# Kernel tuning notes

Measured on AMD Instinct MI355X. Metric: run time of the kernel, lower is better.

The kernel has to match this reference:

```python
import jax, jax.numpy as jnp
import numpy as np

AABB0 = np.array([-1.5, -1.5, -1.5], np.float32)
AABB1 = np.array([1.5, 1.5, 1.5], np.float32)
GRID = (300, 300, 300)
NEAR, FAR = 2.0, 6.0
STEP = float(np.mean((AABB1 - AABB0) / (np.array(GRID, np.float32) - 1)) * 0.5)  # step_ratio=0.5
DIST_SCALE = 25.0
DENSITY_SHIFT = -10.0
W_THRES = 1e-4
PE = 2  # view_pe = feat_pe = 2
MAT = ((0, 1), (0, 2), (1, 2))
VEC = (2, 1, 0)
N_RAYS, N_SAMP = 1024, 512
DN, AN = 16, 16
APP_DIM, FEAT_C = 27, 128
IN_MLP = 2 * PE * 3 + 2 * PE * APP_DIM + 3 + APP_DIM  # 150


def posenc(x, freqs):
    fb = (2.0 ** jnp.arange(freqs)).astype(x.dtype)
    p = (x[..., None] * fb).reshape(x.shape[:-1] + (x.shape[-1] * freqs,))
    return jnp.concatenate([jnp.sin(p), jnp.cos(p)], -1)


def bilinear2d(plane, xy):
    # plane [C,H,W]; xy [P,2] in [-1,1], x->W, y->H; align_corners=True, border clamp
    C, H, W = plane.shape
    x = jnp.clip((xy[:, 0] * 0.5 + 0.5) * (W - 1), 0.0, W - 1)
    y = jnp.clip((xy[:, 1] * 0.5 + 0.5) * (H - 1), 0.0, H - 1)
    x0 = jnp.clip(jnp.floor(x), 0, W - 2).astype(jnp.int32)
    y0 = jnp.clip(jnp.floor(y), 0, H - 2).astype(jnp.int32)
    wx, wy = x - x0, y - y0
    v00 = plane[:, y0, x0]
    v01 = plane[:, y0, x0 + 1]
    v10 = plane[:, y0 + 1, x0]
    v11 = plane[:, y0 + 1, x0 + 1]
    return (v00 * (1 - wx) + v01 * wx) * (1 - wy) + (v10 * (1 - wx) + v11 * wx) * wy  # [C,P]


def linear1d(line, z):
    # line [C,L]; z [P] in [-1,1]
    C, L = line.shape
    t = jnp.clip((z * 0.5 + 0.5) * (L - 1), 0.0, L - 1)
    i0 = jnp.clip(jnp.floor(t), 0, L - 2).astype(jnp.int32)
    w = t - i0
    return line[:, i0] * (1 - w) + line[:, i0 + 1] * w  # [C,P]


def _forward(rays_o, rays_d, dplanes, dlines, aplanes, alines, basis_w,
             w1, b1, w2, b2, w3, b3, n_samples):
    a0, a1 = jnp.asarray(AABB0), jnp.asarray(AABB1)
    # --- sample_ray (is_train=False) ---
    vec = jnp.where(rays_d == 0, 1e-6, rays_d)
    rate_a = (a1 - rays_o) / vec
    rate_b = (a0 - rays_o) / vec
    t_min = jnp.clip(jnp.max(jnp.minimum(rate_a, rate_b), -1), NEAR, FAR)  # [R]
    rng = jnp.arange(n_samples, dtype=rays_o.dtype)[None]
    z_vals = t_min[:, None] + STEP * rng  # [R,S]
    pts = rays_o[:, None, :] + rays_d[:, None, :] * z_vals[..., None]  # [R,S,3]
    ray_valid = jnp.all((pts >= a0) & (pts <= a1), -1)  # [R,S]
    xn = ((pts - a0) * (2.0 / (a1 - a0)) - 1.0).reshape(-1, 3)  # normalize_coord -> [P,3]
    # --- density: VM decomposition (sum of plane*line products) ---
    sigma_feat = jnp.zeros((xn.shape[0],), xn.dtype)
    for i in range(3):
        p = bilinear2d(dplanes[i], xn[:, jnp.array(MAT[i])])
        l = linear1d(dlines[i], xn[:, VEC[i]])
        sigma_feat = sigma_feat + jnp.sum(p * l, 0)
    sigma = jax.nn.softplus(sigma_feat + DENSITY_SHIFT).reshape(z_vals.shape)
    sigma = jnp.where(ray_valid, sigma, 0.0)
    # --- raw2alpha compositing ---
    dists = jnp.concatenate([z_vals[:, 1:] - z_vals[:, :-1], jnp.zeros_like(z_vals[:, :1])], -1)
    alpha = 1.0 - jnp.exp(-sigma * dists * DIST_SCALE)
    T = jnp.cumprod(jnp.concatenate([jnp.ones_like(alpha[:, :1]), 1.0 - alpha + 1e-10], -1), -1)
    weight = alpha * T[:, :-1]
    app_mask = weight > W_THRES
    # --- appearance features + basis_mat ---
    coefs = [bilinear2d(aplanes[i], xn[:, jnp.array(MAT[i])]) * linear1d(alines[i], xn[:, VEC[i]])
             for i in range(3)]
    feat = jnp.concatenate(coefs, 0).T @ basis_w.T  # [P, app_dim]
    view = jnp.broadcast_to(rays_d[:, None, :], pts.shape).reshape(-1, 3)
    # --- MLPRender_Fea: [features, viewdirs, posenc(features), posenc(viewdirs)] ---
    mlp_in = jnp.concatenate([feat, view, posenc(feat, PE), posenc(view, PE)], -1)
    h = jax.nn.relu(mlp_in @ w1.T + b1)
    h = jax.nn.relu(h @ w2.T + b2)
    rgb = jax.nn.sigmoid(h @ w3.T + b3).reshape(z_vals.shape + (3,))
    rgb = jnp.where(app_mask[..., None], rgb, 0.0)
    acc = jnp.sum(weight, -1)
    rgb_map = jnp.sum(weight[..., None] * rgb, 1)
    rgb_map = jnp.clip(rgb_map + (1.0 - acc)[:, None], 0.0, 1.0)  # white background
    depth_map = jnp.sum(weight * z_vals, -1)
    return rgb_map, depth_map


def setup_inputs() -> dict:
    key = jax.random.key(0)
    ks = jax.random.split(key, 20)
    rd = jax.random.normal(ks[0], (N_RAYS, 3), jnp.float32)
    rays_d = rd / jnp.linalg.norm(rd, axis=-1, keepdims=True)
    rays_o = -3.0 * rays_d + 0.1 * jax.random.normal(ks[1], (N_RAYS, 3), jnp.float32)
    inp = {"rays_o": rays_o, "rays_d": rays_d}
    for i, ((m0, m1), v) in enumerate(zip(MAT, VEC)):
        inp[f"dplane{i}"] = jax.random.normal(ks[2 + i], (DN, GRID[m1], GRID[m0]), jnp.float32)
        inp[f"dline{i}"] = jax.random.normal(ks[5 + i], (DN, GRID[v]), jnp.float32)
        inp[f"aplane{i}"] = 0.1 * jax.random.normal(ks[8 + i], (AN, GRID[m1], GRID[m0]), jnp.float32)
        inp[f"aline{i}"] = 0.1 * jax.random.normal(ks[11 + i], (AN, GRID[v]), jnp.float32)
    inp["basis_w"] = 0.1 * jax.random.normal(ks[14], (APP_DIM, 3 * AN), jnp.float32)
    inp["w1"] = 0.05 * jax.random.normal(ks[15], (FEAT_C, IN_MLP), jnp.float32)
    inp["b1"] = jnp.zeros((FEAT_C,), jnp.float32)
    inp["w2"] = 0.05 * jax.random.normal(ks[16], (FEAT_C, FEAT_C), jnp.float32)
    inp["b2"] = jnp.zeros((FEAT_C,), jnp.float32)
    inp["w3"] = 0.05 * jax.random.normal(ks[17], (3, FEAT_C), jnp.float32)
    inp["b3"] = jnp.zeros((3,), jnp.float32)
    inp["n_samples"] = N_SAMP
    return inp


def reference(rays_o, rays_d, dplane0, dplane1, dplane2, dline0, dline1, dline2,
              aplane0, aplane1, aplane2, aline0, aline1, aline2, basis_w,
              w1, b1, w2, b2, w3, b3, n_samples):
    return _forward(rays_o, rays_d, (dplane0, dplane1, dplane2), (dline0, dline1, dline2),
                    (aplane0, aplane1, aplane2), (aline0, aline1, aline2), basis_w,
                    w1, b1, w2, b2, w3, b3, n_samples)
```

## Files before the change

kernel.cpp:

```cpp
#include <hip/hip_runtime.h>
#include <hip/hip_fp16.h>
#include <math.h>

#define NRAYS 1024
#define NSAMP 512
#define GRIDN 300
#define POS_ELEMS (GRIDN*GRIDN)
#define PLANE_ELEMS (16*POS_ELEMS)
#define CMAX 524288

typedef short bf16x8 __attribute__((ext_vector_type(8)));
typedef short short8 __attribute__((ext_vector_type(8)));
typedef float f32x4  __attribute__((ext_vector_type(4)));

struct H8v { __half2 h[4]; };

__device__ __forceinline__ float clampf(float x, float a, float b){ return fminf(fmaxf(x,a),b); }
__device__ __forceinline__ unsigned short f2b(float f){
    unsigned u = __builtin_bit_cast(unsigned, f);
    u = (u + 0x7FFFu + ((u>>16)&1u)) >> 16;
    return (unsigned short)u;
}
__device__ __forceinline__ float b2f(unsigned short h){
    unsigned u = ((unsigned)h) << 16;
    return __builtin_bit_cast(float, u);
}

__device__ __forceinline__ float ray_tmin(float o0,float o1,float o2,float d0,float d1,float d2){
    float v0=(d0==0.f)?1e-6f:d0, v1=(d1==0.f)?1e-6f:d1, v2=(d2==0.f)?1e-6f:d2;
    float t_min = -1e30f, a, b;
    a=(1.5f-o0)/v0; b=(-1.5f-o0)/v0; t_min=fmaxf(t_min,fminf(a,b));
    a=(1.5f-o1)/v1; b=(-1.5f-o1)/v1; t_min=fmaxf(t_min,fminf(a,b));
    a=(1.5f-o2)/v2; b=(-1.5f-o2)/v2; t_min=fmaxf(t_min,fminf(a,b));
    return clampf(t_min, 2.0f, 6.0f);
}

struct TPtrs {
    const float* psrc[6]; __half* pdst[6];
    const float* lsrc[6]; __half* ldst[6];
};

__global__ __launch_bounds__(256) void k_transpose(TPtrs tp) {
    int by  = blockIdx.y;
    int pos = blockIdx.x * 256 + threadIdx.x;
    if (pos < POS_ELEMS) {
        const float* src = tp.psrc[by];
        __half2 o[8];
        #pragma unroll
        for (int e = 0; e < 8; e++) {
            float a = src[(2*e  ) * POS_ELEMS + pos];
            float b = src[(2*e+1) * POS_ELEMS + pos];
            o[e] = __float22half2_rn(make_float2(a,b));
        }
        float4* dst = (float4*)(tp.pdst[by] + (size_t)pos * 16);
        dst[0] = *(float4*)&o[0];
        dst[1] = *(float4*)&o[4];
    }
    if (pos < GRIDN) {
        const float* ls = tp.lsrc[by];
        __half*      ld = tp.ldst[by];
        #pragma unroll
        for (int c = 0; c < 16; c++) ld[pos * 16 + c] = __float2half_rn(ls[c * GRIDN + pos]);
    }
}

__global__ __launch_bounds__(256) void k_prepw(
    const float* __restrict__ w1, const float* __restrict__ w2,
    unsigned short* __restrict__ w1b, unsigned short* __restrict__ w2b)
{
    int idx = blockIdx.x * 256 + threadIdx.x;
    if (idx < 128*160) {
        int j = idx / 160, k = idx - j*160;
        w1b[idx] = (k < 150) ? f2b(w1[j*150 + k]) : 0;
    } else if (idx < 128*160 + 128*128) {
        int i2 = idx - 128*160;
        w2b[i2] = f2b(w2[i2]);
    }
}

__global__ __launch_bounds__(256) void k_alpha(
    const float* __restrict__ ro, const float* __restrict__ rd,
    const __half* __restrict__ dpT0, const __half* __restrict__ dpT1, const __half* __restrict__ dpT2,
    const __half* __restrict__ dlT0, const __half* __restrict__ dlT1, const __half* __restrict__ dlT2,
    float* __restrict__ alpha_out)
{
    const float STEPF = (3.0f/299.0f)*0.5f;
    int gid = blockIdx.x*256 + threadIdx.x;
    int id = gid >> 1, h = gid & 1;
    int r = id >> 9, s = id & (NSAMP-1);

    float o0=ro[r*3+0], o1=ro[r*3+1], o2=ro[r*3+2];
    float d0=rd[r*3+0], d1=rd[r*3+1], d2=rd[r*3+2];
    float t_min = ray_tmin(o0,o1,o2,d0,d1,d2);

    float z  = t_min + STEPF * (float)s;
    float p0 = o0 + d0*z, p1 = o1 + d1*z, p2 = o2 + d2*z;
    bool valid = (p0>=-1.5f)&&(p0<=1.5f)&&(p1>=-1.5f)&&(p1<=1.5f)&&(p2>=-1.5f)&&(p2<=1.5f);

    float sfp = 0.f;
    if (valid) {
        float xn[3] = { (p0+1.5f)*(2.0f/3.0f)-1.0f,
                        (p1+1.5f)*(2.0f/3.0f)-1.0f,
                        (p2+1.5f)*(2.0f/3.0f)-1.0f };
        const __half* dpT[3] = {dpT0,dpT1,dpT2};
        const __half* dlT[3] = {dlT0,dlT1,dlT2};
        const int M0[3]={0,0,1}, M1[3]={1,2,2}, V[3]={2,1,0};
        #pragma unroll
        for (int i=0;i<3;i++) {
            float fx = clampf((xn[M0[i]]*0.5f+0.5f)*299.f, 0.f, 299.f);
            float fy = clampf((xn[M1[i]]*0.5f+0.5f)*299.f, 0.f, 299.f);
            float ft = clampf((xn[V[i]] *0.5f+0.5f)*299.f, 0.f, 299.f);
            int x0=min((int)fx,298), y0=min((int)fy,298), i0=min((int)ft,298);
            float wx=fx-(float)x0, wy=fy-(float)y0, wt=ft-(float)i0;
            __half2 w00=__float2half2_rn((1.f-wx)*(1.f-wy)), w01=__float2half2_rn(wx*(1.f-wy));
            __half2 w10=__float2half2_rn((1.f-wx)*wy),       w11=__float2half2_rn(wx*wy);
            __half2 u0 =__float2half2_rn(1.f-wt),            u1 =__float2half2_rn(wt);
            const __half* base = dpT[i] + (size_t)(y0*GRIDN+x0)*16 + h*8;
            H8v a00 = *(const H8v*)(base);
            H8v a01 = *(const H8v*)(base + 16);
            H8v a10 = *(const H8v*)(base + GRIDN*16);
            H8v a11 = *(const H8v*)(base + GRIDN*16 + 16);
            const __half* lb = dlT[i] + (size_t)i0*16 + h*8;
            H8v l0 = *(const H8v*)(lb);
            H8v l1 = *(const H8v*)(lb + 16);
            #pragma unroll
            for (int e=0;e<4;e++) {
                __half2 p = __hmul2(a00.h[e],w00);
                p = __hfma2(a01.h[e],w01,p);
                p = __hfma2(a10.h[e],w10,p);
                p = __hfma2(a11.h[e],w11,p);
                __half2 l = __hmul2(l0.h[e],u0);
                l = __hfma2(l1.h[e],u1,l);
                float2 c = __half22float2(__hmul2(p,l));
                sfp += c.x + c.y;
            }
        }
    }
    float sf = sfp + __shfl_xor(sfp, 1, 64);
    if (h == 0) {
        float sig = 0.f;
        if (valid) {
            float xs = sf - 10.0f;
            sig = fmaxf(xs, 0.f) + __logf(1.f + __expf(-fabsf(xs)));
        }
        alpha_out[id] = (s < NSAMP-1) ? (1.f - __expf(-sig * (STEPF*25.0f))) : 0.f;
    }
}

__global__ __launch_bounds__(256) void k_scan(
    const float* __restrict__ ro, const float* __restrict__ rd,
    const float* __restrict__ alpha_in,
    float* __restrict__ acc_out, float* __restrict__ depth_out,
    int* __restrict__ tmpl, float* __restrict__ tmpw, int* __restrict__ cnt)
{
    const float STEPF = (3.0f/299.0f)*0.5f;
    int r = blockIdx.x;
    int tid = threadIdx.x;
    int lane = tid & 63, wv = tid >> 6;

    float o0=ro[r*3+0], o1=ro[r*3+1], o2=ro[r*3+2];
    float d0=rd[r*3+0], d1=rd[r*3+1], d2=rd[r*3+2];
    float t_min = ray_tmin(o0,o1,o2,d0,d1,d2);

    float2 av = *(const float2*)&alpha_in[r*NSAMP + 2*tid];
    float aj0 = av.x, aj1 = av.y;
    float zj0 = t_min + STEPF * (float)(2*tid);
    float zj1 = t_min + STEPF * (float)(2*tid+1);

    float v0 = (1.f - aj0) + 1e-10f;
    float v1 = (1.f - aj1) + 1e-10f;
    float inc = v0 * v1;
    #pragma unroll
    for (int off=1; off<64; off<<=1) {
        float t = __shfl_up(inc, off, 64);
        if (lane >= off) inc *= t;
    }
    __shared__ float wtot[4], swsum[4], sdep[4];
    __shared__ int   wcnt[4];
    if (lane == 63) wtot[wv] = inc;
    __syncthreads();
    float pre = 1.f;
    for (int i=0;i<wv;i++) pre *= wtot[i];
    float excl = __shfl_up(inc, 1, 64);
    if (lane == 0) excl = 1.f;
    float T0 = pre * excl;
    float w0 = aj0 * T0;
    float w1 = aj1 * T0 * v0;

    float rw = w0 + w1, rz = w0*zj0 + w1*zj1;
    #pragma unroll
    for (int off=32; off>0; off>>=1) { rw += __shfl_xor(rw,off,64); rz += __shfl_xor(rz,off,64); }
    if (lane == 0) { swsum[wv] = rw; sdep[wv] = rz; }

    bool act0 = (w0 > 1e-4f), act1 = (w1 > 1e-4f);
    unsigned long long m0 = __ballot(act0);
    unsigned long long m1 = __ballot(act1);
    int tot = __popcll(m0) + __popcll(m1);
    if (lane == 0) wcnt[wv] = tot;
    __syncthreads();
    int base = 0;
    for (int i=0;i<wv;i++) base += wcnt[i];
    unsigned long long below = (1ull<<lane)-1ull;
    int o = base + __popcll(m0 & below) + __popcll(m1 & below);
    int* tl = tmpl + r*NSAMP;
    float* tw = tmpw + r*NSAMP;
    if (act0) { tl[o] = (r<<9)|(2*tid);   tw[o] = w0; o++; }
    if (act1) { tl[o] = (r<<9)|(2*tid+1); tw[o] = w1; }

    if (tid == 0) {
        float a=0.f, b=0.f;
        #pragma unroll
        for (int i=0;i<4;i++){ a+=swsum[i]; b+=sdep[i]; }
        acc_out[r] = a; depth_out[r] = b;
        cnt[r] = wcnt[0]+wcnt[1]+wcnt[2]+wcnt[3];
    }
}

__global__ __launch_bounds__(1024) void k_prefix(
    const int* __restrict__ cnt, int* __restrict__ basep, int* __restrict__ counter)
{
    int tid = threadIdx.x;
    int lane = tid & 63, wv = tid >> 6;
    int v = cnt[tid];
    int inc = v;
    #pragma unroll
    for (int off=1; off<64; off<<=1) {
        int t = __shfl_up(inc, off, 64);
        if (lane >= off) inc += t;
    }
    __shared__ int wsum[16];
    if (lane == 63) wsum[wv] = inc;
    __syncthreads();
    int pre = 0;
    for (int i=0;i<wv;i++) pre += wsum[i];
    basep[tid] = pre + inc - v;
    if (tid == 1023) *counter = pre + inc;
}

__global__ __launch_bounds__(256) void k_compact(
    const int* __restrict__ tmpl, const float* __restrict__ tmpw,
    const int* __restrict__ cnt, const int* __restrict__ basep,
    int* __restrict__ list, float* __restrict__ wlist)
{
    int r = blockIdx.x;
    int n = cnt[r], b = basep[r];
    const int* tl = tmpl + r*NSAMP;
    const float* tw = tmpw + r*NSAMP;
    for (int j = threadIdx.x; j < n; j += 256) {
        list[b+j]  = tl[j];
        wlist[b+j] = tw[j];
    }
}

__global__ __launch_bounds__(256) void k_gather(
    const float* __restrict__ ro, const float* __restrict__ rd,
    const __half* __restrict__ apT0, const __half* __restrict__ apT1, const __half* __restrict__ apT2,
    const __half* __restrict__ alT0, const __half* __restrict__ alT1, const __half* __restrict__ alT2,
    const float* __restrict__ basis_w,
    const int* __restrict__ list, const int* __restrict__ counter,
    float* __restrict__ Xf)
{
    const float STEPF = (3.0f/299.0f)*0.5f;
    int gid = blockIdx.x*256 + threadIdx.x;
    int idx = gid >> 3, q = gid & 7;
    int count = *counter;
    if (idx >= count) return;

    int sid = list[idx];
    int r = sid >> 9, s = sid & (NSAMP-1);
    float o0=ro[r*3+0], o1=ro[r*3+1], o2=ro[r*3+2];
    float d0=rd[r*3+0], d1=rd[r*3+1], d2=rd[r*3+2];
    float t_min = ray_tmin(o0,o1,o2,d0,d1,d2);
    float z = t_min + STEPF*(float)s;
    float xn[3] = { ((o0+d0*z)+1.5f)*(2.0f/3.0f)-1.0f,
                    ((o1+d1*z)+1.5f)*(2.0f/3.0f)-1.0f,
                    ((o2+d2*z)+1.5f)*(2.0f/3.0f)-1.0f };

    bool active = (q < 6);
    int i = min(q >> 1, 2);
    int h = q & 1;

    float c8[8];
    {
        const __half* apT[3]={apT0,apT1,apT2};
        const __half* alT[3]={alT0,alT1,alT2};
        const int M0[3]={0,0,1}, M1[3]={1,2,2}, V[3]={2,1,0};
        float fx = clampf((xn[M0[i]]*0.5f+0.5f)*299.f, 0.f, 299.f);
        float fy = clampf((xn[M1[i]]*0.5f+0.5f)*299.f, 0.f, 299.f);
        float ft = clampf((xn[V[i]] *0.5f+0.5f)*299.f, 0.f, 299.f);
        int x0=min((int)fx,298), y0=min((int)fy,298), i0=min((int)ft,298);
        float wx=fx-(float)x0, wy=fy-(float)y0, wt=ft-(float)i0;
        __half2 w00=__float2half2_rn((1.f-wx)*(1.f-wy)), w01=__float2half2_rn(wx*(1.f-wy));
        __half2 w10=__float2half2_rn((1.f-wx)*wy),       w11=__float2half2_rn(wx*wy);
        __half2 u0 =__float2half2_rn(1.f-wt),            u1 =__float2half2_rn(wt);
        if (active) {
            const __half* base = apT[i] + (size_t)(y0*GRIDN+x0)*16 + h*8;
            H8v a00 = *(const H8v*)(base);
            H8v a01 = *(const H8v*)(base + 16);
            H8v a10 = *(const H8v*)(base + GRIDN*16);
            H8v a11 = *(const H8v*)(base + GRIDN*16 + 16);
            const __half* lb = alT[i] + (size_t)i0*16 + h*8;
            H8v l0 = *(const H8v*)(lb);
            H8v l1 = *(const H8v*)(lb + 16);
            #pragma unroll
            for (int e=0;e<4;e++) {
                __half2 p = __hmul2(a00.h[e],w00);
                p = __hfma2(a01.h[e],w01,p);
                p = __hfma2(a10.h[e],w10,p);
                p = __hfma2(a11.h[e],w11,p);
                __half2 l = __hmul2(l0.h[e],u0);
                l = __hfma2(l1.h[e],u1,l);
                float2 c = __half22float2(__hmul2(p,l));
                c8[2*e]   = c.x;
                c8[2*e+1] = c.y;
            }
        } else {
            #pragma unroll
            for (int e=0;e<8;e++) c8[e] = 0.f;
        }
    }

    float kv[4] = {0.f, 0.f, 0.f, 0.f};
    #pragma unroll
    for (int j=0;j<27;j++) {
        const float4* b4 = (const float4*)(basis_w + j*48 + i*16 + h*8);
        float4 b0 = b4[0], b1 = b4[1];
        float p = b0.x*c8[0] + b0.y*c8[1] + b0.z*c8[2] + b0.w*c8[3]
                + b1.x*c8[4] + b1.y*c8[5] + b1.z*c8[6] + b1.w*c8[7];
        p += __shfl_xor(p, 1, 64);
        p += __shfl_xor(p, 2, 64);
        p += __shfl_xor(p, 4, 64);
        if (q == (j >> 2)) kv[j & 3] = p;
    }

    float4 v = make_float4(kv[0], kv[1], kv[2], kv[3]);
    if (q == 6) v.w = d0;
    if (q == 7) { v = make_float4(d1, d2, 0.f, 0.f); }
    *(float4*)&Xf[(size_t)idx*32 + q*4] = v;
}

#define XST 168
#define HST 136
#define TIL 32
#define XFS 36

__global__ __launch_bounds__(512, 4) void k_gemm(
    const float* __restrict__ Xf,
    const unsigned short* __restrict__ w1b, const float* __restrict__ b1p,
    const unsigned short* __restrict__ w2b, const float* __restrict__ b2p,
    const float* __restrict__ w3p, const float* __restrict__ b3p,
    const float* __restrict__ wlist, const int* __restrict__ counter,
    __half* __restrict__ contrib)
{
    __shared__ __align__(16) unsigned short Xs[TIL*XST];
    __shared__ __align__(16) unsigned short Hs[TIL*HST];
    __shared__ __align__(16) float Xf_s[TIL][XFS];

    int tid  = threadIdx.x;
    int wvid = tid >> 6, lane = tid & 63, ln15 = lane & 15, kq = lane >> 4;

    int count  = *counter;
    int ntiles = (count + TIL-1) >> 5;
    if ((int)blockIdx.x >= ntiles) return;

    int jrow = (wvid<<4) + ln15;
    bf16x8 w1f[5], w2f[4];
    #pragma unroll
    for (int ks=0; ks<5; ks++)
        w1f[ks] = *(const bf16x8*)&w1b[jrow*160 + ks*32 + kq*8];
    #pragma unroll
    for (int ks=0; ks<4; ks++)
        w2f[ks] = *(const bf16x8*)&w2b[jrow*128 + ks*32 + kq*8];
    float bias1 = b1p[jrow];
    float bias2 = b2p[jrow];

    for (int t = blockIdx.x; t < ntiles; t += gridDim.x) {
        if (tid < TIL*8) {
            int row = tid >> 3, q = tid & 7;
            int idx = t*TIL + row;
            float4 v = make_float4(0.f,0.f,0.f,0.f);
            if (idx < count) v = *(const float4*)&Xf[(size_t)idx*32 + q*4];
            *(float4*)&Xf_s[row][q*4] = v;
        }
        __syncthreads();

        for (int u = tid; u < TIL*30; u += 512) {
            int row = u / 30, j = u - row*30;
            unsigned short* X = &Xs[row*XST];
            float f = Xf_s[row][j];
            float s1 = __sinf(f), s2 = __sinf(2.f*f);
            float c1 = __cosf(f), c2 = __cosf(2.f*f);
            X[j] = f2b(f);
            int c = j - 27;
            int o_s = (j < 27) ? (30 + 2*j) : (138 + 2*c);
            int o_c = (j < 27) ? (84 + 2*j) : (144 + 2*c);
            X[o_s]   = f2b(s1); X[o_s+1] = f2b(s2);
            X[o_c]   = f2b(c1); X[o_c+1] = f2b(c2);
        }
        for (int u = tid; u < TIL*10; u += 512) {
            int row = u / 10, k = 150 + (u - row*10);
            Xs[row*XST + k] = 0;
        }
        __syncthreads();

        {
            f32x4 acc[2] = {};
            #pragma unroll
            for (int ks=0; ks<5; ks++) {
                int ko = ks*32 + kq*8;
                #pragma unroll
                for (int m=0;m<2;m++) {
                    bf16x8 a = *(const bf16x8*)&Xs[(m*16 + ln15)*XST + ko];
                    acc[m] = __builtin_amdgcn_mfma_f32_16x16x32_bf16(a, w1f[ks], acc[m], 0,0,0);
                }
            }
            int col = jrow;
            #pragma unroll
            for (int m=0;m<2;m++) {
                int rbase = m*16 + kq*4;
                #pragma unroll
                for (int j=0;j<4;j++)
                    Hs[(rbase+j)*HST + col] = f2b(fmaxf(acc[m][j] + bias1, 0.f));
            }
        }
        __syncthreads();

        {
            f32x4 acc[2] = {};
            #pragma unroll
            for (int ks=0; ks<4; ks++) {
                int ko = ks*32 + kq*8;
                #pragma unroll
                for (int m=0;m<2;m++) {
                    bf16x8 a = *(const bf16x8*)&Hs[(m*16 + ln15)*HST + ko];
                    acc[m] = __builtin_amdgcn_mfma_f32_16x16x32_bf16(a, w2f[ks], acc[m], 0,0,0);
                }
            }
            int col = jrow;
            #pragma unroll
            for (int m=0;m<2;m++) {
                int rbase = m*16 + kq*4;
                #pragma unroll
                for (int j=0;j<4;j++)
                    Xs[(rbase+j)*HST + col] = f2b(fmaxf(acc[m][j] + bias2, 0.f));
            }
        }
        __syncthreads();

        if (tid < TIL*8) {
            int u = tid >> 3, q = tid & 7;
            int idx = t*TIL + u;
            if (q < 6 && idx < count) {
                int ch = q >> 1, hf = q & 1;
                float wgt = wlist[idx];
                const unsigned short* h2 = Xs + u*HST + hf*64;
                const float* wr = w3p + ch*128 + hf*64;
                float p = 0.f;
                #pragma unroll
                for (int k=0;k<64;k+=8) {
                    bf16x8 hv = *(const bf16x8*)&h2[k];
                    #pragma unroll
                    for (int e=0;e<8;e++)
                        p += b2f((unsigned short)hv[e]) * wr[k+e];
                }
                p += __shfl_xor(p, 1, 64);
                if (hf == 0) {
                    float v = 0.f;
                    if (wgt > 0.f) {
                        float acc5 = b3p[ch] + p;
                        v = wgt * (1.f/(1.f + __expf(-acc5)));
                    }
                    contrib[(size_t)ch*CMAX + idx] = __float2half(v);
                }
            }
        }
        __syncthreads();
    }
}

__global__ __launch_bounds__(128) void k_rgbsum(
    const __half* __restrict__ contrib,
    const int* __restrict__ cnt, const int* __restrict__ basep,
    float* __restrict__ rgbacc)
{
    int r = blockIdx.x;
    int n = cnt[r], b = basep[r];
    int tid = threadIdx.x, lane = tid & 63, w = tid >> 6;
    float s0=0.f, s1=0.f, s2=0.f;
    for (int j = tid; j < n; j += 128) {
        s0 += __half2float(contrib[0*CMAX + b + j]);
        s1 += __half2float(contrib[1*CMAX + b + j]);
        s2 += __half2float(contrib[2*CMAX + b + j]);
    }
    #pragma unroll
    for (int off=32; off>0; off>>=1) {
        s0 += __shfl_xor(s0,off,64); s1 += __shfl_xor(s1,off,64); s2 += __shfl_xor(s2,off,64);
    }
    __shared__ float sh[3][2];
    if (lane == 0) { sh[0][w]=s0; sh[1][w]=s1; sh[2][w]=s2; }
    __syncthreads();
    if (tid == 0) {
        rgbacc[r*3+0] = sh[0][0]+sh[0][1];
        rgbacc[r*3+1] = sh[1][0]+sh[1][1];
        rgbacc[r*3+2] = sh[2][0]+sh[2][1];
    }
}

__global__ __launch_bounds__(256) void k_final(
    const float* __restrict__ rgbacc, const float* __restrict__ acc_out, float* __restrict__ out)
{
    int i = blockIdx.x*256 + threadIdx.x;
    if (i < NRAYS*3) {
        int r = i/3;
        out[i] = clampf(rgbacc[i] + (1.f - acc_out[r]), 0.f, 1.f);
    }
}

extern "C" void kernel_launch(void* const* d_in, const int* in_sizes, int n_in,
                              void* d_out, int out_size, void* d_ws, size_t ws_size,
                              hipStream_t stream)
{
    const float* ro = (const float*)d_in[0];
    const float* rd = (const float*)d_in[1];
    const float* dplane[3] = {(const float*)d_in[2],(const float*)d_in[6],(const float*)d_in[10]};
    const float* dline[3]  = {(const float*)d_in[3],(const float*)d_in[7],(const float*)d_in[11]};
    const float* aplane[3] = {(const float*)d_in[4],(const float*)d_in[8],(const float*)d_in[12]};
    const float* aline[3]  = {(const float*)d_in[5],(const float*)d_in[9],(const float*)d_in[13]};
    const float* basis_w = (const float*)d_in[14];
    const float* w1 = (const float*)d_in[15];
    const float* b1 = (const float*)d_in[16];
    const float* w2 = (const float*)d_in[17];
    const float* b2 = (const float*)d_in[18];
    const float* w3 = (const float*)d_in[19];
    const float* b3 = (const float*)d_in[20];
    float* out = (float*)d_out;

    char* ws = (char*)d_ws;
    int*    counter  = (int*)   (ws + 0);
    float*  rgbacc   = (float*) (ws + 256);
    float*  accb     = (float*) (ws + 12544);
    float*  wlist    = (float*) (ws + 16640);
    int*    list     = (int*)   (ws + 2113792);
    __half* planesT  = (__half*)(ws + 4210944);
    __half* linesT   = (__half*)(ws + 21490944);
    unsigned short* w1b = (unsigned short*)(ws + 21548544);
    unsigned short* w2b = (unsigned short*)(ws + 21589504);
    float*  alphab   = (float*) (ws + 21622272);
    int*    cntb     = (int*)   (ws + 23719424);
    int*    baseb    = (int*)   (ws + 23723520);
    int*    tmpl     = (int*)   (ws + 23727616);
    float*  tmpw     = (float*) (ws + 25824768);
    __half* contrib  = (__half*)(ws + 23727616);
    float*  Xf       = (float*) (ws + 27921920);


    TPtrs tp;
    for (int i=0;i<3;i++) {
        tp.psrc[i]   = dplane[i]; tp.pdst[i]   = planesT + (size_t)i*PLANE_ELEMS;
        tp.psrc[3+i] = aplane[i]; tp.pdst[3+i] = planesT + (size_t)(3+i)*PLANE_ELEMS;
        tp.lsrc[i]   = dline[i];  tp.ldst[i]   = linesT + i*(GRIDN*16);
        tp.lsrc[3+i] = aline[i];  tp.ldst[3+i] = linesT + (3+i)*(GRIDN*16);
    }
    dim3 tg((POS_ELEMS+255)/256, 6);
    hipLaunchKernelGGL(k_transpose, tg, dim3(256), 0, stream, tp);

    k_prepw<<<(128*160 + 128*128 + 255)/256, 256, 0, stream>>>(w1, w2, w1b, w2b);

    k_alpha<<<(NRAYS*NSAMP*2)/256, 256, 0, stream>>>(
        ro, rd,
        planesT + 0*(size_t)PLANE_ELEMS, planesT + 1*(size_t)PLANE_ELEMS, planesT + 2*(size_t)PLANE_ELEMS,
        linesT + 0*(GRIDN*16), linesT + 1*(GRIDN*16), linesT + 2*(GRIDN*16),
        alphab);

    k_scan<<<NRAYS, 256, 0, stream>>>(
        ro, rd, alphab, accb, out + NRAYS*3, tmpl, tmpw, cntb);

    k_prefix<<<1, 1024, 0, stream>>>(cntb, baseb, counter);

    k_compact<<<NRAYS, 256, 0, stream>>>(tmpl, tmpw, cntb, baseb, list, wlist);

    k_gather<<<(CMAX*8)/256, 256, 0, stream>>>(
        ro, rd,
        planesT + 3*(size_t)PLANE_ELEMS, planesT + 4*(size_t)PLANE_ELEMS, planesT + 5*(size_t)PLANE_ELEMS,
        linesT + 3*(GRIDN*16), linesT + 4*(GRIDN*16), linesT + 5*(GRIDN*16),
        basis_w, list, counter, Xf);

    k_gemm<<<4096, 512, 0, stream>>>(
        Xf, w1b, b1, w2b, b2, w3, b3,
        wlist, counter, contrib);

    k_rgbsum<<<NRAYS, 128, 0, stream>>>(contrib, cntb, baseb, rgbacc);

    k_final<<<(NRAYS*3+255)/256, 256, 0, stream>>>(rgbacc, accb, out);
}
```

Measured before the change: 109.1 us.

## Double-buffer feature tile loads in MLP GEMM kernel with register prefetch

Input features for the next tile are loaded from global memory into registers at the start of each iteration, then written to a second shared-memory buffer after the layer-2 sync. This hides global load latency behind the posenc and MFMA work and removes one barrier per tile. The raw-feature copy into the bf16 input row now writes two values packed into one 32-bit store. It costs extra shared memory and live registers, which could lower occupancy under the 512x4 launch bound.

```diff
diff --git a/kernel.cpp b/kernel.cpp
--- a/kernel.cpp
+++ b/kernel.cpp
@@ -354,7 +354,7 @@
 {
     __shared__ __align__(16) unsigned short Xs[TIL*XST];
     __shared__ __align__(16) unsigned short Hs[TIL*HST];
-    __shared__ __align__(16) float Xf_s[TIL][XFS];
+    __shared__ __align__(16) float Xf_s[2][TIL][XFS];
 
     int tid  = threadIdx.x;
     int wvid = tid >> 6, lane = tid & 63, ln15 = lane & 15, kq = lane >> 4;
@@ -374,28 +374,45 @@
     float bias1 = b1p[jrow];
     float bias2 = b2p[jrow];
 
+    int srow = tid >> 3, sq = tid & 7;
+
+    int cur = 0;
+    {
+        int t0 = blockIdx.x;
+        if (tid < TIL*8) {
+            int idx = t0*TIL + srow;
+            float4 v = make_float4(0.f,0.f,0.f,0.f);
+            if (idx < count) v = *(const float4*)&Xf[(size_t)idx*32 + sq*4];
+            *(float4*)&Xf_s[0][srow][sq*4] = v;
+        }
+        __syncthreads();
+    }
+
     for (int t = blockIdx.x; t < ntiles; t += gridDim.x) {
-        if (tid < TIL*8) {
-            int row = tid >> 3, q = tid & 7;
-            int idx = t*TIL + row;
-            float4 v = make_float4(0.f,0.f,0.f,0.f);
-            if (idx < count) v = *(const float4*)&Xf[(size_t)idx*32 + q*4];
-            *(float4*)&Xf_s[row][q*4] = v;
-        }
-        __syncthreads();
+        int tn = t + gridDim.x;
+        bool havepf = (tn < ntiles) && (tid < TIL*8);
+        float4 pf = make_float4(0.f,0.f,0.f,0.f);
+        if (havepf) {
+            int idx = tn*TIL + srow;
+            if (idx < count) pf = *(const float4*)&Xf[(size_t)idx*32 + sq*4];
+        }
 
         for (int u = tid; u < TIL*30; u += 512) {
             int row = u / 30, j = u - row*30;
             unsigned short* X = &Xs[row*XST];
-            float f = Xf_s[row][j];
+            float f = Xf_s[cur][row][j];
             float s1 = __sinf(f), s2 = __sinf(2.f*f);
             float c1 = __cosf(f), c2 = __cosf(2.f*f);
-            X[j] = f2b(f);
             int c = j - 27;
             int o_s = (j < 27) ? (30 + 2*j) : (138 + 2*c);
             int o_c = (j < 27) ? (84 + 2*j) : (144 + 2*c);
             X[o_s]   = f2b(s1); X[o_s+1] = f2b(s2);
             X[o_c]   = f2b(c1); X[o_c+1] = f2b(c2);
+            if ((j & 1) == 0) {
+                float fB = Xf_s[cur][row][j+1];
+                unsigned pk = (unsigned)f2b(f) | ((unsigned)f2b(fB) << 16);
+                *(unsigned*)&X[j] = pk;
+            }
         }
         for (int u = tid; u < TIL*10; u += 512) {
             int row = u / 10, k = 150 + (u - row*10);
@@ -446,6 +463,9 @@
             }
         }
         __syncthreads();
+
+        if (havepf)
+            *(float4*)&Xf_s[cur^1][srow][sq*4] = pf;
 
         if (tid < TIL*8) {
             int u = tid >> 3, q = tid & 7;
@@ -475,6 +495,7 @@
             }
         }
         __syncthreads();
+        cur ^= 1;
     }
 }
 
```

After: 108.7 us. No clear change (-0.4%).
